# Optimization experiments

Hardware: AMD Instinct MI355X
Metric: run time of the kernel (lower is better)

## Reference

```python
import jax, jax.numpy as jnp
import numpy as np

N_NODES = 100000


def gcn_conv(x, edge_index, W, b):
    """PyG GCNConv: h = x W^T; add self-loops; symmetric deg^-1/2 norm; scatter-add; + bias."""
    n = x.shape[0]
    src = jnp.concatenate([edge_index[0], jnp.arange(n)])  # self-loops appended
    dst = jnp.concatenate([edge_index[1], jnp.arange(n)])
    deg = jax.ops.segment_sum(jnp.ones_like(dst, dtype=x.dtype), dst, num_segments=n)
    dinv = jnp.where(deg > 0, jax.lax.rsqrt(deg), 0.0)
    norm = dinv[src] * dinv[dst]                             # [E+n]
    h = x @ W.T                                              # [n, out]
    msg = norm[:, None] * h[src]                             # [E+n, out] gather
    out = jax.ops.segment_sum(msg, dst, num_segments=n)      # scatter-add
    return out + b


def setup_inputs() -> dict:
    key = jax.random.key(0)
    ks = jax.random.split(key, 10)
    input_dim, gnn_hidden, tree_hidden, num_classes = 128, 64, 32, 8
    n_edges = 3200000
    x = jax.random.normal(ks[0], (N_NODES, input_dim), dtype=jnp.float32)
    edge_index = jax.random.randint(ks[1], (2, n_edges), 0, N_NODES, dtype=jnp.int64)
    # GCNConv params (PyG Linear weight is [out, in], glorot-ish scale)
    W1 = jax.random.normal(ks[2], (gnn_hidden, input_dim), dtype=jnp.float32) / np.sqrt(input_dim)
    b1 = jnp.zeros((gnn_hidden,), dtype=jnp.float32)
    W2 = jax.random.normal(ks[3], (tree_hidden, gnn_hidden), dtype=jnp.float32) / np.sqrt(gnn_hidden)
    b2 = jnp.zeros((tree_hidden,), dtype=jnp.float32)
    # SoftDecisionTree params (torch.randn init in source)
    gate_w = jax.random.normal(ks[4], (tree_hidden, tree_hidden), dtype=jnp.float32)
    gate_b = jnp.zeros((tree_hidden,), dtype=jnp.float32)
    leaf_w = jax.random.normal(ks[5], (tree_hidden, num_classes), dtype=jnp.float32)
    return {"x": x, "edge_index": edge_index, "W1": W1, "b1": b1, "W2": W2,
            "b2": b2, "gate_w": gate_w, "gate_b": gate_b, "leaf_w": leaf_w}


def reference(x, edge_index, W1, b1, W2, b2, gate_w, gate_b, leaf_w):
    h = jax.nn.relu(gcn_conv(x, edge_index, W1, b1))
    h = gcn_conv(h, edge_index, W2, b2)
    gates = jax.nn.sigmoid(h @ gate_w.T + gate_b)
    return gates @ leaf_w
```

## Files before the change

kernel.cpp:

```cpp
#include <hip/hip_runtime.h>
#include <math.h>

#define IN_DIM 128
#define H1 64
#define H2 32
#define NC 8
#define SCAN_CH 1024
#define NB_MAX 512
#define BLK 512
#define CAP 12288

typedef unsigned int u32;

__device__ __forceinline__ float bf_lo(u32 u) { return __uint_as_float(u << 16); }
__device__ __forceinline__ float bf_hi(u32 u) { return __uint_as_float(u & 0xffff0000u); }
__device__ __forceinline__ unsigned short f2b(float f) {
  u32 u = __float_as_uint(f);
  u += 0x7fffu + ((u >> 16) & 1u);
  return (unsigned short)(u >> 16);
}


__global__ __launch_bounds__(256) void k_hist(const int* __restrict__ dst,
                                              int* __restrict__ bh,
                                              int E, int EPB, int NBk) {
  __shared__ int h[NB_MAX];
  int k = blockIdx.x, tid = threadIdx.x;
  for (int i = tid; i < NBk; i += 256) h[i] = 0;
  __syncthreads();
  int st = k * EPB, en = min(E, st + EPB);
  for (int i = st + tid; i < en; i += 256)
    atomicAdd(&h[((u32)dst[i]) >> 8], 1);
  __syncthreads();
  for (int b = tid; b < NBk; b += 256) bh[b * BLK + k] = h[b];
}


__global__ __launch_bounds__(256) void k_gsc1(const int* __restrict__ A,
                                              int* __restrict__ bsum, int L) {
  int b = blockIdx.x, tid = threadIdx.x;
  int i0 = b * SCAN_CH + tid * 4;
  int s = 0;
  if (i0 + 3 < L) {
    int4 v = *(const int4*)(A + i0);
    s = v.x + v.y + v.z + v.w;
  } else {
    for (int i = i0; i < L; ++i) s += A[i];
  }
  __shared__ int red[256];
  red[tid] = s;
  __syncthreads();
  for (int d = 128; d > 0; d >>= 1) {
    if (tid < d) red[tid] += red[tid + d];
    __syncthreads();
  }
  if (tid == 0) bsum[b] = red[0];
}

__global__ __launch_bounds__(256) void k_gsc2(const int* __restrict__ bsum,
                                              int* __restrict__ bbase,
                                              int* __restrict__ S, int nbk, int L) {
  __shared__ int part[256];
  int tid = threadIdx.x;
  int chunk = (nbk + 255) / 256;
  int st = tid * chunk, en = min(st + chunk, nbk);
  int s = 0;
  for (int i = st; i < en; ++i) s += bsum[i];
  part[tid] = s;
  __syncthreads();
  for (int d = 1; d < 256; d <<= 1) {
    int t = (tid >= d) ? part[tid - d] : 0;
    __syncthreads();
    part[tid] += t;
    __syncthreads();
  }
  int base = (tid == 0) ? 0 : part[tid - 1];
  for (int i = st; i < en; ++i) { bbase[i] = base; base += bsum[i]; }
  if (tid == 255) S[L] = part[255];
}

__global__ __launch_bounds__(256) void k_gsc3(const int* __restrict__ A,
                                              const int* __restrict__ bbase,
                                              int* __restrict__ S, int L) {
  int b = blockIdx.x, tid = threadIdx.x;
  int i0 = b * SCAN_CH + tid * 4;
  int e0 = 0, e1 = 0, e2 = 0, e3 = 0;
  if (i0 + 3 < L) {
    int4 v = *(const int4*)(A + i0);
    e0 = v.x; e1 = v.y; e2 = v.z; e3 = v.w;
  } else {
    if (i0 + 0 < L) e0 = A[i0 + 0];
    if (i0 + 1 < L) e1 = A[i0 + 1];
    if (i0 + 2 < L) e2 = A[i0 + 2];
    if (i0 + 3 < L) e3 = A[i0 + 3];
  }
  __shared__ int part[256];
  part[tid] = e0 + e1 + e2 + e3;
  __syncthreads();
  for (int d = 1; d < 256; d <<= 1) {
    int t = (tid >= d) ? part[tid - d] : 0;
    __syncthreads();
    part[tid] += t;
    __syncthreads();
  }
  int base = bbase[b] + ((tid == 0) ? 0 : part[tid - 1]);
  int o0 = base, o1 = o0 + e0, o2 = o1 + e1, o3 = o2 + e2;
  if (i0 + 3 < L) {
    int4 o; o.x = o0; o.y = o1; o.z = o2; o.w = o3;
    *(int4*)(S + i0) = o;
  } else {
    if (i0 + 0 < L) S[i0 + 0] = o0;
    if (i0 + 1 < L) S[i0 + 1] = o1;
    if (i0 + 2 < L) S[i0 + 2] = o2;
    if (i0 + 3 < L) S[i0 + 3] = o3;
  }
}


__global__ __launch_bounds__(256) void k_scatter(const int* __restrict__ src,
                                                 const int* __restrict__ dst,
                                                 const int* __restrict__ S,
                                                 u32* __restrict__ packed,
                                                 int E, int EPB, int NBk) {
  __shared__ int cur[NB_MAX];
  int k = blockIdx.x, tid = threadIdx.x;
  for (int b = tid; b < NBk; b += 256) cur[b] = S[b * BLK + k];
  __syncthreads();
  int st = k * EPB, en = min(E, st + EPB);
  for (int i = st + tid; i < en; i += 256) {
    int d = dst[i];
    int b = ((u32)d) >> 8;
    int pos = atomicAdd(&cur[b], 1);
    packed[pos] = (((u32)d & 255u) << 17) | (u32)src[i];
  }
}


__global__ __launch_bounds__(256) void k_build(const u32* __restrict__ packed,
                                               const int* __restrict__ S,
                                               int* __restrict__ csr,
                                               int* __restrict__ off,
                                               float* __restrict__ dinv,
                                               int n, int NBk) {
  __shared__ int cnt[256];
  __shared__ int tmp[256];
  __shared__ int cur[256];
  __shared__ int sbuf[CAP];
  int b = blockIdx.x, tid = threadIdx.x;
  int r0 = S[b * BLK];
  int r1 = S[(b + 1) * BLK];
  int m = r1 - r0;
  cnt[tid] = 0;
  __syncthreads();
  for (int i = r0 + tid; i < r1; i += 256)
    atomicAdd(&cnt[packed[i] >> 17], 1);
  __syncthreads();
  int v = cnt[tid];
  tmp[tid] = v;
  __syncthreads();
  for (int d = 1; d < 256; d <<= 1) {
    int t = (tid >= d) ? tmp[tid - d] : 0;
    __syncthreads();
    tmp[tid] += t;
    __syncthreads();
  }
  int rel = tmp[tid] - v;
  int node = b * 256 + tid;
  if (node < n) {
    off[node] = r0 + rel;
    dinv[node] = rsqrtf((float)(v + 1));
  }
  if (b == NBk - 1 && tid == 0) off[n] = r1;
  cur[tid] = rel;
  __syncthreads();
  if (m <= CAP) {
    for (int i = r0 + tid; i < r1; i += 256) {
      u32 u = packed[i];
      int pos = atomicAdd(&cur[u >> 17], 1);
      sbuf[pos] = (int)(u & 0x1FFFFu);
    }
    __syncthreads();
    for (int j = tid; j < m; j += 256)
      csr[r0 + j] = sbuf[j];
  } else {
    for (int i = r0 + tid; i < r1; i += 256) {
      u32 u = packed[i];
      int pos = atomicAdd(&cur[u >> 17], 1);
      csr[r0 + pos] = (int)(u & 0x1FFFFu);
    }
  }
}


__global__ void k_proj1(const float4* __restrict__ x4, const float* __restrict__ W1,
                        const float* __restrict__ dinv,
                        unsigned short* __restrict__ h1p, int n) {
  __shared__ float xs[16][IN_DIM];
  __shared__ float wt[IN_DIM][H1 + 1];
  int tid = threadIdx.x;
  int row0 = blockIdx.x * 16;

  for (int i = tid; i < (H1 * IN_DIM / 4); i += 256) {
    float4 w = ((const float4*)W1)[i];
    int o = (i * 4) / IN_DIM;
    int k = (i * 4) % IN_DIM;
    wt[k + 0][o] = w.x; wt[k + 1][o] = w.y; wt[k + 2][o] = w.z; wt[k + 3][o] = w.w;
  }
  for (int i = tid; i < 16 * IN_DIM / 4; i += 256) {
    int r = (i * 4) / IN_DIM, k = (i * 4) % IN_DIM;
    int row = row0 + r;
    if (row < n)
      *((float4*)&xs[r][k]) = x4[(size_t)row * (IN_DIM / 4) + k / 4];
  }
  __syncthreads();

  int o = tid & 63, rq = tid >> 6;
  float a0 = 0.f, a1 = 0.f, a2 = 0.f, a3 = 0.f;
  for (int k = 0; k < IN_DIM; ++k) {
    float w = wt[k][o];
    a0 += xs[rq * 4 + 0][k] * w;
    a1 += xs[rq * 4 + 1][k] * w;
    a2 += xs[rq * 4 + 2][k] * w;
    a3 += xs[rq * 4 + 3][k] * w;
  }
  int r = row0 + rq * 4;
  if (r + 0 < n) h1p[(size_t)(r + 0) * H1 + o] = f2b(a0 * dinv[r + 0]);
  if (r + 1 < n) h1p[(size_t)(r + 1) * H1 + o] = f2b(a1 * dinv[r + 1]);
  if (r + 2 < n) h1p[(size_t)(r + 2) * H1 + o] = f2b(a2 * dinv[r + 2]);
  if (r + 3 < n) h1p[(size_t)(r + 3) * H1 + o] = f2b(a3 * dinv[r + 3]);
}


#define ACC8(v) do { \
    a0 += bf_lo((v).x); a1 += bf_hi((v).x); \
    a2 += bf_lo((v).y); a3 += bf_hi((v).y); \
    a4 += bf_lo((v).z); a5 += bf_hi((v).z); \
    a6 += bf_lo((v).w); a7 += bf_hi((v).w); } while (0)

#define RED8(m) do { \
    a0 += __shfl_xor(a0, m, 64); a1 += __shfl_xor(a1, m, 64); \
    a2 += __shfl_xor(a2, m, 64); a3 += __shfl_xor(a3, m, 64); \
    a4 += __shfl_xor(a4, m, 64); a5 += __shfl_xor(a5, m, 64); \
    a6 += __shfl_xor(a6, m, 64); a7 += __shfl_xor(a7, m, 64); } while (0)

__global__ __launch_bounds__(256) void k_agg64_proj2(
    const u32* __restrict__ hp,
    const float* __restrict__ dinv,
    const int* __restrict__ off, const int* __restrict__ csr,
    const float* __restrict__ b1, const float* __restrict__ W2,
    unsigned short* __restrict__ h2p, int n) {
  __shared__ float wt[H1][H2 + 1];
  __shared__ float rows[4][H1];
  __shared__ float b1s[H1];
  int tid = threadIdx.x;

  for (int i = tid; i < H2 * H1 / 4; i += 256) {
    float4 w = ((const float4*)W2)[i];
    int o = (i * 4) / H1, k = (i * 4) % H1;
    wt[k + 0][o] = w.x; wt[k + 1][o] = w.y; wt[k + 2][o] = w.z; wt[k + 3][o] = w.w;
  }
  if (tid < 16) ((float4*)b1s)[tid] = ((const float4*)b1)[tid];
  __syncthreads();

  int lane = tid & 63;
  int wv = __builtin_amdgcn_readfirstlane(tid >> 6);
  int wid0 = blockIdx.x * 4 + wv;
  int wid = wid0 < n ? wid0 : n - 1;
  int g = lane >> 3, j = lane & 7;

  const uint4* __restrict__ hp4 = (const uint4*)hp;
  float a0 = 0.f, a1 = 0.f, a2 = 0.f, a3 = 0.f,
        a4 = 0.f, a5 = 0.f, a6 = 0.f, a7 = 0.f;

  if (g == 0) {
    uint4 v = hp4[(size_t)wid * (H1 / 8) + j];
    ACC8(v);
  }
  int r0 = off[wid], r1 = off[wid + 1];
  for (int base = r0; base < r1; base += 32) {
    int ci = base + (lane & 31);
    int s = csr[min(ci, r1 - 1)];
#pragma unroll
    for (int it = 0; it < 4; ++it) {
      int sv = __shfl(s, it * 8 + g, 64);
      if (base + it * 8 + g < r1) {
        uint4 v = hp4[(size_t)sv * (H1 / 8) + j];
        ACC8(v);
      }
    }
  }
  RED8(8); RED8(16); RED8(32);

  float d = dinv[wid];
  if (lane < 8) {
    float4 v0, v1;
    v0.x = fmaxf(a0 * d + b1s[8 * lane + 0], 0.f);
    v0.y = fmaxf(a1 * d + b1s[8 * lane + 1], 0.f);
    v0.z = fmaxf(a2 * d + b1s[8 * lane + 2], 0.f);
    v0.w = fmaxf(a3 * d + b1s[8 * lane + 3], 0.f);
    v1.x = fmaxf(a4 * d + b1s[8 * lane + 4], 0.f);
    v1.y = fmaxf(a5 * d + b1s[8 * lane + 5], 0.f);
    v1.z = fmaxf(a6 * d + b1s[8 * lane + 6], 0.f);
    v1.w = fmaxf(a7 * d + b1s[8 * lane + 7], 0.f);
    *(float4*)&rows[wv][8 * lane + 0] = v0;
    *(float4*)&rows[wv][8 * lane + 4] = v1;
  }
  __syncthreads();

  int half = lane >> 5, o = lane & 31;
  float a = 0.f;
#pragma unroll
  for (int k = 0; k < 32; ++k) {
    int kk = half * 32 + k;
    a += rows[wv][kk] * wt[kk][o];
  }
  a += __shfl_down(a, 32, 64);
  if (half == 0 && wid0 < n) h2p[(size_t)wid0 * H2 + o] = f2b(a * d);
}


__global__ __launch_bounds__(256) void k_agg32_tree(
    const u32* __restrict__ hp,
    const float* __restrict__ dinv,
    const int* __restrict__ off, const int* __restrict__ csr,
    const float* __restrict__ b2, const float* __restrict__ gate_w,
    const float* __restrict__ gate_b, const float* __restrict__ leaf_w,
    float* __restrict__ out, int n) {
  __shared__ float gwt[H2][H2 + 1];
  __shared__ float lws[H2][NC + 1];
  __shared__ float rowh[4][H2];
  __shared__ float rowg[4][H2];
  __shared__ float b2s[H2];
  int tid = threadIdx.x;

  {
    float4 w = ((const float4*)gate_w)[tid];
    int jj = (tid * 4) / H2, k = (tid * 4) % H2;
    gwt[k + 0][jj] = w.x; gwt[k + 1][jj] = w.y; gwt[k + 2][jj] = w.z; gwt[k + 3][jj] = w.w;
  }
  lws[tid >> 3][tid & 7] = leaf_w[tid];
  if (tid < 8) ((float4*)b2s)[tid] = ((const float4*)b2)[tid];
  __syncthreads();

  int lane = tid & 63;
  int wv = __builtin_amdgcn_readfirstlane(tid >> 6);
  int wid0 = blockIdx.x * 4 + wv;
  int wid = wid0 < n ? wid0 : n - 1;
  int g = lane >> 2, j = lane & 3;

  const uint4* __restrict__ hp4 = (const uint4*)hp;
  float a0 = 0.f, a1 = 0.f, a2 = 0.f, a3 = 0.f,
        a4 = 0.f, a5 = 0.f, a6 = 0.f, a7 = 0.f;

  if (g == 0) {
    uint4 v = hp4[(size_t)wid * (H2 / 8) + j];
    ACC8(v);
  }
  int r0 = off[wid], r1 = off[wid + 1];
  for (int base = r0; base < r1; base += 32) {
    int ci = base + (lane & 31);
    int s = csr[min(ci, r1 - 1)];
#pragma unroll
    for (int it = 0; it < 2; ++it) {
      int sv = __shfl(s, it * 16 + g, 64);
      if (base + it * 16 + g < r1) {
        uint4 v = hp4[(size_t)sv * (H2 / 8) + j];
        ACC8(v);
      }
    }
  }
  RED8(4); RED8(8); RED8(16); RED8(32);

  float d = dinv[wid];
  if (lane < 4) {
    float4 v0, v1;
    v0.x = a0 * d + b2s[8 * lane + 0];
    v0.y = a1 * d + b2s[8 * lane + 1];
    v0.z = a2 * d + b2s[8 * lane + 2];
    v0.w = a3 * d + b2s[8 * lane + 3];
    v1.x = a4 * d + b2s[8 * lane + 4];
    v1.y = a5 * d + b2s[8 * lane + 5];
    v1.z = a6 * d + b2s[8 * lane + 6];
    v1.w = a7 * d + b2s[8 * lane + 7];
    *(float4*)&rowh[wv][8 * lane + 0] = v0;
    *(float4*)&rowh[wv][8 * lane + 4] = v1;
  }
  __syncthreads();

  int half = lane >> 5, f = lane & 31;
  float gacc = 0.f;
#pragma unroll
  for (int k = 0; k < 16; ++k) {
    int kk = half * 16 + k;
    gacc += rowh[wv][kk] * gwt[kk][f];
  }
  gacc += __shfl_down(gacc, 32, 64);
  if (half == 0) rowg[wv][f] = 1.0f / (1.0f + __expf(-(gacc + gate_b[f])));
  __syncthreads();

  int c = lane & 7, gi = lane >> 3;
  float a = 0.f;
#pragma unroll
  for (int j4 = 0; j4 < 4; ++j4) {
    int jj = gi * 4 + j4;
    a += rowg[wv][jj] * lws[jj][c];
  }
  a += __shfl_down(a, 32, 64);
  a += __shfl_down(a, 16, 64);
  a += __shfl_down(a, 8, 64);
  if (lane < 8 && wid0 < n) out[(size_t)wid0 * NC + lane] = a;
}


static inline size_t align256(size_t x) { return (x + 255) & ~(size_t)255; }

extern "C" void kernel_launch(void* const* d_in, const int* in_sizes, int n_in,
                              void* d_out, int out_size, void* d_ws, size_t ws_size,
                              hipStream_t stream) {
  const float* x  = (const float*)d_in[0];
  const int*   ei = (const int*)d_in[1];
  const float* W1 = (const float*)d_in[2];
  const float* b1 = (const float*)d_in[3];
  const float* W2 = (const float*)d_in[4];
  const float* b2 = (const float*)d_in[5];
  const float* gw = (const float*)d_in[6];
  const float* gb = (const float*)d_in[7];
  const float* lw = (const float*)d_in[8];
  float* out = (float*)d_out;

  int n = in_sizes[0] / IN_DIM;
  int E = in_sizes[1] / 2;
  const int* src  = ei;
  const int* dstp = ei + E;

  int NBk = (n + 255) >> 8;
  int EPB = (E + BLK - 1) / BLK;
  int L   = NBk * BLK;
  int nbs = (L + SCAN_CH - 1) / SCAN_CH;

  char* w = (char*)d_ws;
  unsigned short* h1p = (unsigned short*)w;  w += align256((size_t)n * H1 * 2);
  unsigned short* h2p = (unsigned short*)w;  w += align256((size_t)n * H2 * 2);
  int* csr    = (int*)w;   w += align256((size_t)E * 4);
  u32* packed = (u32*)w;   w += align256((size_t)E * 4);
  int* bh     = (int*)w;   w += align256(((size_t)L + 1) * 4);
  int* S      = (int*)w;   w += align256(((size_t)L + 1) * 4);
  int* bsum   = (int*)w;   w += align256((size_t)nbs * 4);
  int* bbase  = (int*)w;   w += align256((size_t)nbs * 4);
  float* dinv = (float*)w; w += align256((size_t)n * 4);
  int* off    = (int*)w;   w += align256(((size_t)n + 1) * 4);

  int gw4 = (n + 3) / 4;

  k_hist<<<BLK, 256, 0, stream>>>(dstp, bh, E, EPB, NBk);
  k_gsc1<<<nbs, 256, 0, stream>>>(bh, bsum, L);
  k_gsc2<<<1, 256, 0, stream>>>(bsum, bbase, S, nbs, L);
  k_gsc3<<<nbs, 256, 0, stream>>>(bh, bbase, S, L);
  k_scatter<<<BLK, 256, 0, stream>>>(src, dstp, S, packed, E, EPB, NBk);
  k_build<<<NBk, 256, 0, stream>>>(packed, S, csr, off, dinv, n, NBk);

  k_proj1<<<(n + 15) / 16, 256, 0, stream>>>((const float4*)x, W1, dinv, h1p, n);
  k_agg64_proj2<<<gw4, 256, 0, stream>>>((const u32*)h1p, dinv, off, csr, b1, W2, h2p, n);
  k_agg32_tree<<<gw4, 256, 0, stream>>>((const u32*)h2p, dinv, off, csr, b2, gw, gb, lw, out, n);
}
```

Before: 378.3 us.

## Process two destination nodes per wavefront in both aggregation kernels

Each 64-lane wavefront in the two aggregation kernels now handles two destination nodes, each on its own half-wave. Blocks are halved, and offsets and dinv are loaded once per wave and broadcast by shuffle. The gather loop covers 16 edges per node per iteration, so each node gets fewer lanes per edge batch and the loop runs as long as the larger of the two degrees. The intent is better lane utilization for average degree around 32 and less per-node fixed overhead (launch, weight staging, reductions). The cost is divergence when the two degrees differ.

```diff
diff --git a/kernel.cpp b/kernel.cpp
--- a/kernel.cpp
+++ b/kernel.cpp
@@ -250,7 +250,7 @@
     const float* __restrict__ b1, const float* __restrict__ W2,
     unsigned short* __restrict__ h2p, int n) {
   __shared__ float wt[H1][H2 + 1];
-  __shared__ float rows[4][H1];
+  __shared__ float rows[4][2][H1];
   __shared__ float b1s[H1];
   int tid = threadIdx.x;
 
@@ -264,58 +264,73 @@
 
   int lane = tid & 63;
   int wv = __builtin_amdgcn_readfirstlane(tid >> 6);
-  int wid0 = blockIdx.x * 4 + wv;
-  int wid = wid0 < n ? wid0 : n - 1;
+  int p0n = (blockIdx.x * 4 + wv) * 2;
+  int p0c = min(p0n, n - 1);
+  int p1c = min(p0n + 1, n - 1);
   int g = lane >> 3, j = lane & 7;
+  int nh = g >> 2;
+
+  int tt = 0;
+  if (lane < 3) tt = off[min(p0n + lane, n)];
+  int r00 = __shfl(tt, 0, 64);
+  int r01 = __shfl(tt, 1, 64);
+  int r11 = __shfl(tt, 2, 64);
+  float dv = 0.f;
+  if (lane < 2) dv = dinv[min(p0n + lane, n - 1)];
+  float d0 = __shfl(dv, 0, 64), d1 = __shfl(dv, 1, 64);
 
   const uint4* __restrict__ hp4 = (const uint4*)hp;
   float a0 = 0.f, a1 = 0.f, a2 = 0.f, a3 = 0.f,
         a4 = 0.f, a5 = 0.f, a6 = 0.f, a7 = 0.f;
 
-  if (g == 0) {
-    uint4 v = hp4[(size_t)wid * (H1 / 8) + j];
+  if ((g & 3) == 0) {
+    uint4 v = hp4[(size_t)(nh ? p1c : p0c) * (H1 / 8) + j];
     ACC8(v);
   }
-  int r0 = off[wid], r1 = off[wid + 1];
-  for (int base = r0; base < r1; base += 32) {
-    int ci = base + (lane & 31);
-    int s = csr[min(ci, r1 - 1)];
+
+  int mx = max(r01 - r00, r11 - r01);
+  for (int kk = 0; kk * 16 < mx; ++kk) {
+    int b0 = r00 + 16 * kk, b1e = r01 + 16 * kk;
+    int ci = (lane < 32) ? min(b0 + (lane & 15), r01 - 1)
+                         : min(b1e + (lane & 15), r11 - 1);
+    int s = csr[max(ci, 0)];
 #pragma unroll
     for (int it = 0; it < 4; ++it) {
-      int sv = __shfl(s, it * 8 + g, 64);
-      if (base + it * 8 + g < r1) {
+      int e = it * 4 + (g & 3);
+      int sv = __shfl(s, (nh ? 32 : 0) + e, 64);
+      int eidx = (nh ? b1e : b0) + e;
+      int lim = nh ? r11 : r01;
+      if (eidx < lim) {
         uint4 v = hp4[(size_t)sv * (H1 / 8) + j];
         ACC8(v);
       }
     }
   }
-  RED8(8); RED8(16); RED8(32);
-
-  float d = dinv[wid];
-  if (lane < 8) {
+  RED8(8); RED8(16);
+
+  float d = (lane < 32) ? d0 : d1;
+  if ((lane & 31) < 8) {
+    int jj = lane & 7, nn = lane >> 5;
     float4 v0, v1;
-    v0.x = fmaxf(a0 * d + b1s[8 * lane + 0], 0.f);
-    v0.y = fmaxf(a1 * d + b1s[8 * lane + 1], 0.f);
-    v0.z = fmaxf(a2 * d + b1s[8 * lane + 2], 0.f);
-    v0.w = fmaxf(a3 * d + b1s[8 * lane + 3], 0.f);
-    v1.x = fmaxf(a4 * d + b1s[8 * lane + 4], 0.f);
-    v1.y = fmaxf(a5 * d + b1s[8 * lane + 5], 0.f);
-    v1.z = fmaxf(a6 * d + b1s[8 * lane + 6], 0.f);
-    v1.w = fmaxf(a7 * d + b1s[8 * lane + 7], 0.f);
-    *(float4*)&rows[wv][8 * lane + 0] = v0;
-    *(float4*)&rows[wv][8 * lane + 4] = v1;
-  }
-  __syncthreads();
-
-  int half = lane >> 5, o = lane & 31;
+    v0.x = fmaxf(a0 * d + b1s[8 * jj + 0], 0.f);
+    v0.y = fmaxf(a1 * d + b1s[8 * jj + 1], 0.f);
+    v0.z = fmaxf(a2 * d + b1s[8 * jj + 2], 0.f);
+    v0.w = fmaxf(a3 * d + b1s[8 * jj + 3], 0.f);
+    v1.x = fmaxf(a4 * d + b1s[8 * jj + 4], 0.f);
+    v1.y = fmaxf(a5 * d + b1s[8 * jj + 5], 0.f);
+    v1.z = fmaxf(a6 * d + b1s[8 * jj + 6], 0.f);
+    v1.w = fmaxf(a7 * d + b1s[8 * jj + 7], 0.f);
+    *(float4*)&rows[wv][nn][8 * jj + 0] = v0;
+    *(float4*)&rows[wv][nn][8 * jj + 4] = v1;
+  }
+  __syncthreads();
+
+  int node = lane >> 5, o = lane & 31;
   float a = 0.f;
 #pragma unroll
-  for (int k = 0; k < 32; ++k) {
-    int kk = half * 32 + k;
-    a += rows[wv][kk] * wt[kk][o];
-  }
-  a += __shfl_down(a, 32, 64);
-  if (half == 0 && wid0 < n) h2p[(size_t)wid0 * H2 + o] = f2b(a * d);
+  for (int k = 0; k < H1; ++k) a += rows[wv][node][k] * wt[k][o];
+  int wout = p0n + node;
+  if (wout < n) h2p[(size_t)wout * H2 + o] = f2b(a * ((node) ? d1 : d0));
 }
 
 
@@ -328,8 +343,8 @@
     float* __restrict__ out, int n) {
   __shared__ float gwt[H2][H2 + 1];
   __shared__ float lws[H2][NC + 1];
-  __shared__ float rowh[4][H2];
-  __shared__ float rowg[4][H2];
+  __shared__ float rowh[4][2][H2];
+  __shared__ float rowg[4][2][H2];
   __shared__ float b2s[H2];
   int tid = threadIdx.x;
 
@@ -344,71 +359,85 @@
 
   int lane = tid & 63;
   int wv = __builtin_amdgcn_readfirstlane(tid >> 6);
-  int wid0 = blockIdx.x * 4 + wv;
-  int wid = wid0 < n ? wid0 : n - 1;
+  int p0n = (blockIdx.x * 4 + wv) * 2;
+  int p0c = min(p0n, n - 1);
+  int p1c = min(p0n + 1, n - 1);
   int g = lane >> 2, j = lane & 3;
+  int nh = g >> 3;
+
+  int tt = 0;
+  if (lane < 3) tt = off[min(p0n + lane, n)];
+  int r00 = __shfl(tt, 0, 64);
+  int r01 = __shfl(tt, 1, 64);
+  int r11 = __shfl(tt, 2, 64);
+  float dv = 0.f;
+  if (lane < 2) dv = dinv[min(p0n + lane, n - 1)];
+  float d0 = __shfl(dv, 0, 64), d1 = __shfl(dv, 1, 64);
 
   const uint4* __restrict__ hp4 = (const uint4*)hp;
   float a0 = 0.f, a1 = 0.f, a2 = 0.f, a3 = 0.f,
         a4 = 0.f, a5 = 0.f, a6 = 0.f, a7 = 0.f;
 
-  if (g == 0) {
-    uint4 v = hp4[(size_t)wid * (H2 / 8) + j];
+  if ((g & 7) == 0) {
+    uint4 v = hp4[(size_t)(nh ? p1c : p0c) * (H2 / 8) + j];
     ACC8(v);
   }
-  int r0 = off[wid], r1 = off[wid + 1];
-  for (int base = r0; base < r1; base += 32) {
-    int ci = base + (lane & 31);
-    int s = csr[min(ci, r1 - 1)];
+
+  int mx = max(r01 - r00, r11 - r01);
+  for (int kk = 0; kk * 16 < mx; ++kk) {
+    int b0 = r00 + 16 * kk, b1e = r01 + 16 * kk;
+    int ci = (lane < 32) ? min(b0 + (lane & 15), r01 - 1)
+                         : min(b1e + (lane & 15), r11 - 1);
+    int s = csr[max(ci, 0)];
 #pragma unroll
     for (int it = 0; it < 2; ++it) {
-      int sv = __shfl(s, it * 16 + g, 64);
-      if (base + it * 16 + g < r1) {
+      int e = it * 8 + (g & 7);
+      int sv = __shfl(s, (nh ? 32 : 0) + e, 64);
+      int eidx = (nh ? b1e : b0) + e;
+      int lim = nh ? r11 : r01;
+      if (eidx < lim) {
         uint4 v = hp4[(size_t)sv * (H2 / 8) + j];
         ACC8(v);
       }
     }
   }
-  RED8(4); RED8(8); RED8(16); RED8(32);
-
-  float d = dinv[wid];
-  if (lane < 4) {
+  RED8(4); RED8(8); RED8(16);
+
+  float d = (lane < 32) ? d0 : d1;
+  if ((lane & 31) < 4) {
+    int jj = lane & 3, nn = lane >> 5;
     float4 v0, v1;
-    v0.x = a0 * d + b2s[8 * lane + 0];
-    v0.y = a1 * d + b2s[8 * lane + 1];
-    v0.z = a2 * d + b2s[8 * lane + 2];
-    v0.w = a3 * d + b2s[8 * lane + 3];
-    v1.x = a4 * d + b2s[8 * lane + 4];
-    v1.y = a5 * d + b2s[8 * lane + 5];
-    v1.z = a6 * d + b2s[8 * lane + 6];
-    v1.w = a7 * d + b2s[8 * lane + 7];
-    *(float4*)&rowh[wv][8 * lane + 0] = v0;
-    *(float4*)&rowh[wv][8 * lane + 4] = v1;
-  }
-  __syncthreads();
-
-  int half = lane >> 5, f = lane & 31;
+    v0.x = a0 * d + b2s[8 * jj + 0];
+    v0.y = a1 * d + b2s[8 * jj + 1];
+    v0.z = a2 * d + b2s[8 * jj + 2];
+    v0.w = a3 * d + b2s[8 * jj + 3];
+    v1.x = a4 * d + b2s[8 * jj + 4];
+    v1.y = a5 * d + b2s[8 * jj + 5];
+    v1.z = a6 * d + b2s[8 * jj + 6];
+    v1.w = a7 * d + b2s[8 * jj + 7];
+    *(float4*)&rowh[wv][nn][8 * jj + 0] = v0;
+    *(float4*)&rowh[wv][nn][8 * jj + 4] = v1;
+  }
+  __syncthreads();
+
+  int node = lane >> 5, f = lane & 31;
   float gacc = 0.f;
 #pragma unroll
-  for (int k = 0; k < 16; ++k) {
-    int kk = half * 16 + k;
-    gacc += rowh[wv][kk] * gwt[kk][f];
-  }
-  gacc += __shfl_down(gacc, 32, 64);
-  if (half == 0) rowg[wv][f] = 1.0f / (1.0f + __expf(-(gacc + gate_b[f])));
-  __syncthreads();
-
-  int c = lane & 7, gi = lane >> 3;
+  for (int k = 0; k < H2; ++k) gacc += rowh[wv][node][k] * gwt[k][f];
+  rowg[wv][node][f] = 1.0f / (1.0f + __expf(-(gacc + gate_b[f])));
+  __syncthreads();
+
+  int c = lane & 7, gi = (lane >> 3) & 3;
   float a = 0.f;
 #pragma unroll
-  for (int j4 = 0; j4 < 4; ++j4) {
-    int jj = gi * 4 + j4;
-    a += rowg[wv][jj] * lws[jj][c];
-  }
-  a += __shfl_down(a, 32, 64);
-  a += __shfl_down(a, 16, 64);
-  a += __shfl_down(a, 8, 64);
-  if (lane < 8 && wid0 < n) out[(size_t)wid0 * NC + lane] = a;
+  for (int j8 = 0; j8 < 8; ++j8) {
+    int jj = gi * 8 + j8;
+    a += rowg[wv][node][jj] * lws[jj][c];
+  }
+  a += __shfl_xor(a, 8, 64);
+  a += __shfl_xor(a, 16, 64);
+  int wout = p0n + node;
+  if ((lane & 31) < 8 && wout < n) out[(size_t)wout * NC + c] = a;
 }
 
 
@@ -450,7 +479,7 @@
   float* dinv = (float*)w; w += align256((size_t)n * 4);
   int* off    = (int*)w;   w += align256(((size_t)n + 1) * 4);
 
-  int gw4 = (n + 3) / 4;
+  int gw8 = (n + 7) / 8;
 
   k_hist<<<BLK, 256, 0, stream>>>(dstp, bh, E, EPB, NBk);
   k_gsc1<<<nbs, 256, 0, stream>>>(bh, bsum, L);
@@ -460,6 +489,6 @@
   k_build<<<NBk, 256, 0, stream>>>(packed, S, csr, off, dinv, n, NBk);
 
   k_proj1<<<(n + 15) / 16, 256, 0, stream>>>((const float4*)x, W1, dinv, h1p, n);
-  k_agg64_proj2<<<gw4, 256, 0, stream>>>((const u32*)h1p, dinv, off, csr, b1, W2, h2p, n);
-  k_agg32_tree<<<gw4, 256, 0, stream>>>((const u32*)h2p, dinv, off, csr, b2, gw, gb, lw, out, n);
-}
+  k_agg64_proj2<<<gw8, 256, 0, stream>>>((const u32*)h1p, dinv, off, csr, b1, W2, h2p, n);
+  k_agg32_tree<<<gw8, 256, 0, stream>>>((const u32*)h2p, dinv, off, csr, b2, gw, gb, lw, out, n);
+}
```

Result: faster. 350.9 us (-7.2%).

## Process four nodes per wavefront in both aggregation kernels

Applied to the files above, without the earlier changes.

Both aggregation kernels now assign four destination nodes to each 64-lane wavefront instead of one. A single coalesced load fetches the CSR offsets and dinv values for all four nodes, each node's neighbours are gathered by a quarter of the wave, and the post-aggregation projections loop over the four nodes. With about 32 neighbours per node, this cuts grid size and per-node setup overhead and reduces the cross-lane reductions. In exchange, the loop runs to the largest degree among the four nodes, so lanes idle when degrees differ, and the per-block shared memory grows.

```diff
diff --git a/kernel.cpp b/kernel.cpp
--- a/kernel.cpp
+++ b/kernel.cpp
@@ -250,7 +250,7 @@
     const float* __restrict__ b1, const float* __restrict__ W2,
     unsigned short* __restrict__ h2p, int n) {
   __shared__ float wt[H1][H2 + 1];
-  __shared__ float rows[4][H1];
+  __shared__ float rows[4][4][H1];
   __shared__ float b1s[H1];
   int tid = threadIdx.x;
 
@@ -264,58 +264,79 @@
 
   int lane = tid & 63;
   int wv = __builtin_amdgcn_readfirstlane(tid >> 6);
-  int wid0 = blockIdx.x * 4 + wv;
-  int wid = wid0 < n ? wid0 : n - 1;
+  int p0 = (blockIdx.x * 4 + wv) * 4;
   int g = lane >> 3, j = lane & 7;
+  int nh = g >> 1, gg = g & 1;
+
+  int tt = 0;
+  if (lane < 5) tt = off[min(p0 + lane, n)];
+  int r0 = __shfl(tt, 0, 64), r1 = __shfl(tt, 1, 64), r2 = __shfl(tt, 2, 64),
+      r3 = __shfl(tt, 3, 64), r4 = __shfl(tt, 4, 64);
+  float dv = 0.f;
+  if (lane < 4) dv = dinv[min(p0 + lane, n - 1)];
+  float d0 = __shfl(dv, 0, 64), d1 = __shfl(dv, 1, 64),
+        d2 = __shfl(dv, 2, 64), d3 = __shfl(dv, 3, 64);
+
+  int rB = (nh == 0) ? r1 : (nh == 1) ? r2 : (nh == 2) ? r3 : r4;
+  int rA = (nh == 0) ? r0 : (nh == 1) ? r1 : (nh == 2) ? r2 : r3;
+  int mydeg = rB - rA;
+  float dN = (nh == 0) ? d0 : (nh == 1) ? d1 : (nh == 2) ? d2 : d3;
+
+  int ln = lane >> 4, pos = lane & 15;
+  int cA = (ln == 0) ? r0 : (ln == 1) ? r1 : (ln == 2) ? r2 : r3;
+  int cB = (ln == 0) ? r1 : (ln == 1) ? r2 : (ln == 2) ? r3 : r4;
 
   const uint4* __restrict__ hp4 = (const uint4*)hp;
   float a0 = 0.f, a1 = 0.f, a2 = 0.f, a3 = 0.f,
         a4 = 0.f, a5 = 0.f, a6 = 0.f, a7 = 0.f;
 
-  if (g == 0) {
-    uint4 v = hp4[(size_t)wid * (H1 / 8) + j];
+  if (gg == 0) {
+    uint4 v = hp4[(size_t)min(p0 + nh, n - 1) * (H1 / 8) + j];
     ACC8(v);
   }
-  int r0 = off[wid], r1 = off[wid + 1];
-  for (int base = r0; base < r1; base += 32) {
-    int ci = base + (lane & 31);
-    int s = csr[min(ci, r1 - 1)];
-#pragma unroll
-    for (int it = 0; it < 4; ++it) {
-      int sv = __shfl(s, it * 8 + g, 64);
-      if (base + it * 8 + g < r1) {
+
+  int mx = max(max(r1 - r0, r2 - r1), max(r3 - r2, r4 - r3));
+  for (int kk = 0; kk * 16 < mx; ++kk) {
+    int ci = cA + 16 * kk + pos;
+    ci = max(min(ci, cB - 1), 0);
+    int s = csr[ci];
+#pragma unroll
+    for (int it = 0; it < 8; ++it) {
+      int e = it * 2 + gg;
+      int sv = __shfl(s, nh * 16 + e, 64);
+      if (16 * kk + e < mydeg) {
         uint4 v = hp4[(size_t)sv * (H1 / 8) + j];
         ACC8(v);
       }
     }
   }
-  RED8(8); RED8(16); RED8(32);
-
-  float d = dinv[wid];
-  if (lane < 8) {
+  RED8(8);
+
+  if (gg == 0) {
     float4 v0, v1;
-    v0.x = fmaxf(a0 * d + b1s[8 * lane + 0], 0.f);
-    v0.y = fmaxf(a1 * d + b1s[8 * lane + 1], 0.f);
-    v0.z = fmaxf(a2 * d + b1s[8 * lane + 2], 0.f);
-    v0.w = fmaxf(a3 * d + b1s[8 * lane + 3], 0.f);
-    v1.x = fmaxf(a4 * d + b1s[8 * lane + 4], 0.f);
-    v1.y = fmaxf(a5 * d + b1s[8 * lane + 5], 0.f);
-    v1.z = fmaxf(a6 * d + b1s[8 * lane + 6], 0.f);
-    v1.w = fmaxf(a7 * d + b1s[8 * lane + 7], 0.f);
-    *(float4*)&rows[wv][8 * lane + 0] = v0;
-    *(float4*)&rows[wv][8 * lane + 4] = v1;
-  }
-  __syncthreads();
-
-  int half = lane >> 5, o = lane & 31;
-  float a = 0.f;
-#pragma unroll
-  for (int k = 0; k < 32; ++k) {
-    int kk = half * 32 + k;
-    a += rows[wv][kk] * wt[kk][o];
-  }
-  a += __shfl_down(a, 32, 64);
-  if (half == 0 && wid0 < n) h2p[(size_t)wid0 * H2 + o] = f2b(a * d);
+    v0.x = fmaxf(a0 * dN + b1s[8 * j + 0], 0.f);
+    v0.y = fmaxf(a1 * dN + b1s[8 * j + 1], 0.f);
+    v0.z = fmaxf(a2 * dN + b1s[8 * j + 2], 0.f);
+    v0.w = fmaxf(a3 * dN + b1s[8 * j + 3], 0.f);
+    v1.x = fmaxf(a4 * dN + b1s[8 * j + 4], 0.f);
+    v1.y = fmaxf(a5 * dN + b1s[8 * j + 5], 0.f);
+    v1.z = fmaxf(a6 * dN + b1s[8 * j + 6], 0.f);
+    v1.w = fmaxf(a7 * dN + b1s[8 * j + 7], 0.f);
+    *(float4*)&rows[wv][nh][8 * j + 0] = v0;
+    *(float4*)&rows[wv][nh][8 * j + 4] = v1;
+  }
+  __syncthreads();
+
+  int o = lane & 31;
+#pragma unroll
+  for (int t = 0; t < 2; ++t) {
+    int node = (lane >> 5) + 2 * t;
+    float a = 0.f;
+#pragma unroll
+    for (int k = 0; k < H1; ++k) a += rows[wv][node][k] * wt[k][o];
+    float dd = (node == 0) ? d0 : (node == 1) ? d1 : (node == 2) ? d2 : d3;
+    if (p0 + node < n) h2p[(size_t)(p0 + node) * H2 + o] = f2b(a * dd);
+  }
 }
 
 
@@ -328,8 +349,8 @@
     float* __restrict__ out, int n) {
   __shared__ float gwt[H2][H2 + 1];
   __shared__ float lws[H2][NC + 1];
-  __shared__ float rowh[4][H2];
-  __shared__ float rowg[4][H2];
+  __shared__ float rowh[4][4][H2];
+  __shared__ float rowg[4][2][H2];
   __shared__ float b2s[H2];
   int tid = threadIdx.x;
 
@@ -344,71 +365,91 @@
 
   int lane = tid & 63;
   int wv = __builtin_amdgcn_readfirstlane(tid >> 6);
-  int wid0 = blockIdx.x * 4 + wv;
-  int wid = wid0 < n ? wid0 : n - 1;
+  int p0 = (blockIdx.x * 4 + wv) * 4;
   int g = lane >> 2, j = lane & 3;
+  int nh = g >> 2, gg = g & 3;
+
+  int tt = 0;
+  if (lane < 5) tt = off[min(p0 + lane, n)];
+  int r0 = __shfl(tt, 0, 64), r1 = __shfl(tt, 1, 64), r2 = __shfl(tt, 2, 64),
+      r3 = __shfl(tt, 3, 64), r4 = __shfl(tt, 4, 64);
+  float dv = 0.f;
+  if (lane < 4) dv = dinv[min(p0 + lane, n - 1)];
+  float d0 = __shfl(dv, 0, 64), d1 = __shfl(dv, 1, 64),
+        d2 = __shfl(dv, 2, 64), d3 = __shfl(dv, 3, 64);
+
+  int rB = (nh == 0) ? r1 : (nh == 1) ? r2 : (nh == 2) ? r3 : r4;
+  int rA = (nh == 0) ? r0 : (nh == 1) ? r1 : (nh == 2) ? r2 : r3;
+  int mydeg = rB - rA;
+  float dN = (nh == 0) ? d0 : (nh == 1) ? d1 : (nh == 2) ? d2 : d3;
+
+  int ln = lane >> 4, pos = lane & 15;
+  int cA = (ln == 0) ? r0 : (ln == 1) ? r1 : (ln == 2) ? r2 : r3;
+  int cB = (ln == 0) ? r1 : (ln == 1) ? r2 : (ln == 2) ? r3 : r4;
 
   const uint4* __restrict__ hp4 = (const uint4*)hp;
   float a0 = 0.f, a1 = 0.f, a2 = 0.f, a3 = 0.f,
         a4 = 0.f, a5 = 0.f, a6 = 0.f, a7 = 0.f;
 
-  if (g == 0) {
-    uint4 v = hp4[(size_t)wid * (H2 / 8) + j];
+  if (gg == 0) {
+    uint4 v = hp4[(size_t)min(p0 + nh, n - 1) * (H2 / 8) + j];
     ACC8(v);
   }
-  int r0 = off[wid], r1 = off[wid + 1];
-  for (int base = r0; base < r1; base += 32) {
-    int ci = base + (lane & 31);
-    int s = csr[min(ci, r1 - 1)];
-#pragma unroll
-    for (int it = 0; it < 2; ++it) {
-      int sv = __shfl(s, it * 16 + g, 64);
-      if (base + it * 16 + g < r1) {
+
+  int mx = max(max(r1 - r0, r2 - r1), max(r3 - r2, r4 - r3));
+  for (int kk = 0; kk * 16 < mx; ++kk) {
+    int ci = cA + 16 * kk + pos;
+    ci = max(min(ci, cB - 1), 0);
+    int s = csr[ci];
+#pragma unroll
+    for (int it = 0; it < 4; ++it) {
+      int e = it * 4 + gg;
+      int sv = __shfl(s, nh * 16 + e, 64);
+      if (16 * kk + e < mydeg) {
         uint4 v = hp4[(size_t)sv * (H2 / 8) + j];
         ACC8(v);
       }
     }
   }
-  RED8(4); RED8(8); RED8(16); RED8(32);
-
-  float d = dinv[wid];
-  if (lane < 4) {
+  RED8(4); RED8(8);
+
+  if (gg == 0) {
     float4 v0, v1;
-    v0.x = a0 * d + b2s[8 * lane + 0];
-    v0.y = a1 * d + b2s[8 * lane + 1];
-    v0.z = a2 * d + b2s[8 * lane + 2];
-    v0.w = a3 * d + b2s[8 * lane + 3];
-    v1.x = a4 * d + b2s[8 * lane + 4];
-    v1.y = a5 * d + b2s[8 * lane + 5];
-    v1.z = a6 * d + b2s[8 * lane + 6];
-    v1.w = a7 * d + b2s[8 * lane + 7];
-    *(float4*)&rowh[wv][8 * lane + 0] = v0;
-    *(float4*)&rowh[wv][8 * lane + 4] = v1;
-  }
-  __syncthreads();
-
-  int half = lane >> 5, f = lane & 31;
-  float gacc = 0.f;
-#pragma unroll
-  for (int k = 0; k < 16; ++k) {
-    int kk = half * 16 + k;
-    gacc += rowh[wv][kk] * gwt[kk][f];
-  }
-  gacc += __shfl_down(gacc, 32, 64);
-  if (half == 0) rowg[wv][f] = 1.0f / (1.0f + __expf(-(gacc + gate_b[f])));
-  __syncthreads();
-
-  int c = lane & 7, gi = lane >> 3;
-  float a = 0.f;
-#pragma unroll
-  for (int j4 = 0; j4 < 4; ++j4) {
-    int jj = gi * 4 + j4;
-    a += rowg[wv][jj] * lws[jj][c];
-  }
-  a += __shfl_down(a, 32, 64);
-  a += __shfl_down(a, 16, 64);
-  a += __shfl_down(a, 8, 64);
-  if (lane < 8 && wid0 < n) out[(size_t)wid0 * NC + lane] = a;
+    v0.x = a0 * dN + b2s[8 * j + 0];
+    v0.y = a1 * dN + b2s[8 * j + 1];
+    v0.z = a2 * dN + b2s[8 * j + 2];
+    v0.w = a3 * dN + b2s[8 * j + 3];
+    v1.x = a4 * dN + b2s[8 * j + 4];
+    v1.y = a5 * dN + b2s[8 * j + 5];
+    v1.z = a6 * dN + b2s[8 * j + 6];
+    v1.w = a7 * dN + b2s[8 * j + 7];
+    *(float4*)&rowh[wv][nh][8 * j + 0] = v0;
+    *(float4*)&rowh[wv][nh][8 * j + 4] = v1;
+  }
+  __syncthreads();
+
+#pragma unroll
+  for (int t = 0; t < 2; ++t) {
+    int node = (lane >> 5) + 2 * t;
+    int f = lane & 31;
+    float gacc = 0.f;
+#pragma unroll
+    for (int k = 0; k < H2; ++k) gacc += rowh[wv][node][k] * gwt[k][f];
+    rowg[wv][lane >> 5][f] = 1.0f / (1.0f + __expf(-(gacc + gate_b[f])));
+    __syncthreads();
+
+    int c = lane & 7, gi = (lane >> 3) & 3;
+    float a = 0.f;
+#pragma unroll
+    for (int j8 = 0; j8 < 8; ++j8) {
+      int jj = gi * 8 + j8;
+      a += rowg[wv][lane >> 5][jj] * lws[jj][c];
+    }
+    a += __shfl_xor(a, 8, 64);
+    a += __shfl_xor(a, 16, 64);
+    if ((lane & 31) < 8 && p0 + node < n) out[(size_t)(p0 + node) * NC + c] = a;
+    __syncthreads();
+  }
 }
 
 
@@ -450,7 +491,7 @@
   float* dinv = (float*)w; w += align256((size_t)n * 4);
   int* off    = (int*)w;   w += align256(((size_t)n + 1) * 4);
 
-  int gw4 = (n + 3) / 4;
+  int gw16 = (n + 15) / 16;
 
   k_hist<<<BLK, 256, 0, stream>>>(dstp, bh, E, EPB, NBk);
   k_gsc1<<<nbs, 256, 0, stream>>>(bh, bsum, L);
@@ -460,6 +501,6 @@
   k_build<<<NBk, 256, 0, stream>>>(packed, S, csr, off, dinv, n, NBk);
 
   k_proj1<<<(n + 15) / 16, 256, 0, stream>>>((const float4*)x, W1, dinv, h1p, n);
-  k_agg64_proj2<<<gw4, 256, 0, stream>>>((const u32*)h1p, dinv, off, csr, b1, W2, h2p, n);
-  k_agg32_tree<<<gw4, 256, 0, stream>>>((const u32*)h2p, dinv, off, csr, b2, gw, gb, lw, out, n);
-}
+  k_agg64_proj2<<<gw16, 256, 0, stream>>>((const u32*)h1p, dinv, off, csr, b1, W2, h2p, n);
+  k_agg32_tree<<<gw16, 256, 0, stream>>>((const u32*)h2p, dinv, off, csr, b2, gw, gb, lw, out, n);
+}
```

Result: faster. 347.8 us (-8.1%).
